# Kernel optimization log

Hardware: AMD Instinct MI355X
Metric: run time of the kernel (lower is better)

## Reference

```python
import jax, jax.numpy as jnp
import numpy as np

N, E, D, H = 50000, 640000, 128, 8
d = D // H  # per-head dim


def layernorm(x, g, b, eps=1e-5):
    mu = jnp.mean(x, axis=-1, keepdims=True)
    var = jnp.var(x, axis=-1, keepdims=True)
    return (x - mu) * jax.lax.rsqrt(var + eps) * g + b


def setup_inputs() -> dict:
    key = jax.random.key(0)
    ks = jax.random.split(key, 14)
    s = 0.05
    return {
        "node_emb": jax.random.normal(ks[0], (N, D), jnp.float32),
        "bond_emb": jax.random.normal(ks[1], (E, D), jnp.float32),
        "basic_attn": jax.random.uniform(ks[2], (E,), jnp.float32),
        "src": jax.random.randint(ks[3], (E,), 0, N),
        "dst": jax.random.randint(ks[4], (E,), 0, N),
        "Wk": jax.random.normal(ks[5], (D, D), jnp.float32) * s,
        "Wq": jax.random.normal(ks[6], (D, D), jnp.float32) * s,
        "Wv": jax.random.normal(ks[7], (D, D), jnp.float32) * s,
        "W_dis": jax.random.normal(ks[8], (1, H), jnp.float32) * s,
        "W_beta": jax.random.normal(ks[9], (3 * D, 1), jnp.float32) * s,
        "ln1_g": jnp.ones((D,), jnp.float32),
        "ln1_b": jnp.zeros((D,), jnp.float32),
        "W_ff1": jax.random.normal(ks[10], (D, 2 * D), jnp.float32) * s,
        "W_ff2": jax.random.normal(ks[11], (2 * D, D), jnp.float32) * s,
    }


def reference(node_emb, bond_emb, basic_attn, src, dst, Wk, Wq, Wv, W_dis,
              W_beta, ln1_g, ln1_b, W_ff1, W_ff2):
    n = node_emb.shape[0]
    # Q/K/V projections (eval mode: dropouts are identity)
    k = (node_emb @ Wk).reshape(n, H, d)
    q = (node_emb @ Wq).reshape(n, H, d)
    v = (bond_emb @ Wv).reshape(-1, H, d)          # per-edge values [E,H,d]
    # per-edge dot-product score (fn.u_dot_v) scaled by sqrt(out_feat)
    scores = jnp.einsum('ehd,ehd->eh', k[src], q[dst])
    scores = scores / jnp.sqrt(jnp.asarray(d, scores.dtype))
    # learned distance decay: Linear(1,H) on basic_attn
    dist = basic_attn[:, None] @ W_dis             # [E,H]
    logits = scores + dist
    # edge_softmax over in-edges of each destination node, per head
    mx = jax.ops.segment_max(logits, dst, num_segments=n)
    mx = jnp.where(jnp.isfinite(mx), mx, 0.0)
    e = jnp.exp(logits - mx[dst])
    den = jax.ops.segment_sum(e, dst, num_segments=n)
    att = e / (den[dst] + 1e-16)                   # [E,H]
    # message = v * att, scatter-sum to destination nodes
    ft = jax.ops.segment_sum(v * att[:, :, None], dst, num_segments=n)
    he = ft.reshape(n, D)
    # beta gating
    beta = jax.nn.sigmoid(
        jnp.concatenate([he, node_emb, he - node_emb], axis=-1) @ W_beta)
    he = beta * node_emb + (1.0 - beta) * he
    # FFN with pre-LN and identity-initialized post-LN
    h = layernorm(he, ln1_g, ln1_b)
    out = jax.nn.relu(h @ W_ff1) @ W_ff2
    ones = jnp.ones((D,), he.dtype)
    zeros = jnp.zeros((D,), he.dtype)
    return layernorm(out + he, ones, zeros)
```

## Files before the change

kernel.cpp:

```cpp
#include <hip/hip_runtime.h>
#include <math.h>

#define NN 50000
#define NE 640000
#define DIM 128
#define NH 8

typedef unsigned short u16;
typedef __attribute__((ext_vector_type(8))) short short8;
typedef __attribute__((ext_vector_type(4))) float f32x4;

__device__ __forceinline__ float wave_sum64(float v) {
  #pragma unroll
  for (int m = 32; m >= 1; m >>= 1) v += __shfl_xor(v, m, 64);
  return v;
}
__device__ __forceinline__ unsigned bf16pk(float a, float b) {
  unsigned ua = __float_as_uint(a); ua = (ua + 0x7fffu + ((ua >> 16) & 1u)) >> 16;
  unsigned ub = __float_as_uint(b); ub = (ub + 0x7fffu + ((ub >> 16) & 1u)) & 0xffff0000u;
  return ua | ub;
}
__device__ __forceinline__ u16 bf16c(float x) {
  unsigned u = __float_as_uint(x);
  return (u16)((u + 0x7fffu + ((u >> 16) & 1u)) >> 16);
}
__device__ __forceinline__ float bf_lo(unsigned v) { return __uint_as_float(v << 16); }
__device__ __forceinline__ float bf_hi(unsigned v) { return __uint_as_float(v & 0xffff0000u); }

#define AS1(p) ((const __attribute__((address_space(1))) unsigned*)(p))
#define AS3(p) ((__attribute__((address_space(3))) unsigned*)(p))

__global__ __launch_bounds__(256) void csr_count_k(const int* __restrict__ dst,
                                                   int* __restrict__ deg) {
  int e = blockIdx.x * 256 + threadIdx.x;
  if (e < NE) atomicAdd(&deg[dst[e]], 1);
}

#define SCAN_T 1024
#define SCHUNK 49
__global__ __launch_bounds__(1024) void scan_k(const int* __restrict__ deg,
                                               int* __restrict__ off,
                                               int* __restrict__ cursor) {
  __shared__ int part[SCAN_T];
  int t = threadIdx.x;
  int lo = t * SCHUNK, hi = lo + SCHUNK; if (hi > NN) hi = NN;
  int s = 0;
  for (int i = lo; i < hi; ++i) s += deg[i];
  part[t] = s;
  __syncthreads();
  for (int o = 1; o < SCAN_T; o <<= 1) {
    int v = (t >= o) ? part[t - o] : 0;
    __syncthreads();
    part[t] += v;
    __syncthreads();
  }
  int base = (t == 0) ? 0 : part[t - 1];
  for (int i = lo; i < hi; ++i) {
    off[i] = base; cursor[i] = base; base += deg[i];
  }
  if (t == SCAN_T - 1) off[NN] = part[SCAN_T - 1];
}

__global__ __launch_bounds__(256) void csr_fill_k(const int* __restrict__ dst,
                                                  int* __restrict__ cursor,
                                                  int* __restrict__ eids,
                                                  int* __restrict__ perm) {
  int e = blockIdx.x * 256 + threadIdx.x;
  if (e < NE) {
    int p = atomicAdd(&cursor[dst[e]], 1);
    eids[p] = e;
    perm[e] = p;
  }
}

__global__ __launch_bounds__(256) void cvt_node_k(const float* __restrict__ x,
                                                  unsigned* __restrict__ o) {
  int t = blockIdx.x * 256 + threadIdx.x;
  if (t < NN * 64) {
    float2 v = *(const float2*)(x + (size_t)2 * t);
    o[t] = bf16pk(v.x, v.y);
  }
}

__global__ __launch_bounds__(256) void wprep_k(const float* __restrict__ W,
                                               u16* __restrict__ Wt,
                                               int K, int N) {
  int t = blockIdx.x * 256 + threadIdx.x;
  if (t < K * N) {
    int n = t / K, k = t - n * K;
    Wt[t] = bf16c(W[(size_t)k * N + n]);
  }
}

__global__ __launch_bounds__(256) void qk_mfma_k(
    const u16* __restrict__ A, const u16* __restrict__ Wtq,
    const u16* __restrict__ Wtk, u16* __restrict__ qo,
    u16* __restrict__ ko) {
  __shared__ u16 At[64 * 128];
  const int wid = threadIdx.x >> 6, l = threadIdx.x & 63;
  const int quad = l >> 4, l16 = l & 15;
  const int c0 = (wid & 1) * 64;
  const u16* wt = (wid < 2) ? Wtq : Wtk;
  u16* ob = (wid < 2) ? qo : ko;
  short8 bfr[4][4];
  #pragma unroll
  for (int ct = 0; ct < 4; ++ct)
    #pragma unroll
    for (int ks = 0; ks < 4; ++ks)
      bfr[ct][ks] = *(const short8*)(wt + (c0 + ct * 16 + l16) * 128 + ks * 32 + quad * 8);
  const int ntiles = (NN + 63) / 64;
  for (int t = blockIdx.x; t < ntiles; t += gridDim.x) {
    const char* gsrc = (const char*)A + (size_t)t * 64 * 128 * 2;
    #pragma unroll
    for (int i = 0; i < 4; ++i) {
      int off = wid * 4096 + i * 1024;
      __builtin_amdgcn_global_load_lds(AS1(gsrc + off + l * 16),
                                       AS3((char*)At + off), 16, 0, 0);
    }
    __syncthreads();
    f32x4 acc[4][4];
    #pragma unroll
    for (int rt = 0; rt < 4; ++rt)
      #pragma unroll
      for (int ct = 0; ct < 4; ++ct)
        acc[rt][ct] = (f32x4){0.f, 0.f, 0.f, 0.f};
    #pragma unroll
    for (int ks = 0; ks < 4; ++ks) {
      short8 af[4];
      #pragma unroll
      for (int rt = 0; rt < 4; ++rt)
        af[rt] = *(const short8*)(At + (rt * 16 + l16) * 128 + ks * 32 + quad * 8);
      #pragma unroll
      for (int rt = 0; rt < 4; ++rt)
        #pragma unroll
        for (int ct = 0; ct < 4; ++ct)
          acc[rt][ct] = __builtin_amdgcn_mfma_f32_16x16x32_bf16(
              af[rt], bfr[ct][ks], acc[rt][ct], 0, 0, 0);
    }
    __syncthreads();
    #pragma unroll
    for (int rt = 0; rt < 4; ++rt)
      #pragma unroll
      for (int r = 0; r < 4; ++r) {
        int row = t * 64 + rt * 16 + quad * 4 + r;
        if (row < NN) {
          u16* op = ob + (size_t)row * 128 + c0 + l16;
          #pragma unroll
          for (int ct = 0; ct < 4; ++ct) op[ct * 16] = bf16c(acc[rt][ct][r]);
        }
      }
  }
}

__global__ __launch_bounds__(256) void ff1_mfma_k(
    const u16* __restrict__ A, const u16* __restrict__ Wt,
    u16* __restrict__ O) {
  __shared__ u16 At[64 * 128];
  const int wid = threadIdx.x >> 6, l = threadIdx.x & 63;
  const int quad = l >> 4, l16 = l & 15;
  const int c0 = wid * 64;
  short8 bfr[4][4];
  #pragma unroll
  for (int ct = 0; ct < 4; ++ct)
    #pragma unroll
    for (int ks = 0; ks < 4; ++ks)
      bfr[ct][ks] = *(const short8*)(Wt + (c0 + ct * 16 + l16) * 128 + ks * 32 + quad * 8);
  const int ntiles = (NN + 63) / 64;
  for (int t = blockIdx.x; t < ntiles; t += gridDim.x) {
    const char* gsrc = (const char*)A + (size_t)t * 64 * 128 * 2;
    #pragma unroll
    for (int i = 0; i < 4; ++i) {
      int off = wid * 4096 + i * 1024;
      __builtin_amdgcn_global_load_lds(AS1(gsrc + off + l * 16),
                                       AS3((char*)At + off), 16, 0, 0);
    }
    __syncthreads();
    f32x4 acc[4][4];
    #pragma unroll
    for (int rt = 0; rt < 4; ++rt)
      #pragma unroll
      for (int ct = 0; ct < 4; ++ct)
        acc[rt][ct] = (f32x4){0.f, 0.f, 0.f, 0.f};
    #pragma unroll
    for (int ks = 0; ks < 4; ++ks) {
      short8 af[4];
      #pragma unroll
      for (int rt = 0; rt < 4; ++rt)
        af[rt] = *(const short8*)(At + (rt * 16 + l16) * 128 + ks * 32 + quad * 8);
      #pragma unroll
      for (int rt = 0; rt < 4; ++rt)
        #pragma unroll
        for (int ct = 0; ct < 4; ++ct)
          acc[rt][ct] = __builtin_amdgcn_mfma_f32_16x16x32_bf16(
              af[rt], bfr[ct][ks], acc[rt][ct], 0, 0, 0);
    }
    __syncthreads();
    #pragma unroll
    for (int rt = 0; rt < 4; ++rt)
      #pragma unroll
      for (int r = 0; r < 4; ++r) {
        int row = t * 64 + rt * 16 + quad * 4 + r;
        if (row < NN) {
          u16* op = O + (size_t)row * 256 + c0 + l16;
          #pragma unroll
          for (int ct = 0; ct < 4; ++ct)
            op[ct * 16] = bf16c(fmaxf(acc[rt][ct][r], 0.f));
        }
      }
  }
}

__global__ __launch_bounds__(256) void ff2_mfma_k(
    const u16* __restrict__ A, const u16* __restrict__ Wt,
    const float* __restrict__ he, float* __restrict__ Z) {
  __shared__ u16 At[64 * 256];
  const int wid = threadIdx.x >> 6, l = threadIdx.x & 63;
  const int quad = l >> 4, l16 = l & 15;
  const int c0 = wid * 32;
  short8 bfr[2][8];
  #pragma unroll
  for (int ct = 0; ct < 2; ++ct)
    #pragma unroll
    for (int ks = 0; ks < 8; ++ks)
      bfr[ct][ks] = *(const short8*)(Wt + (c0 + ct * 16 + l16) * 256 + ks * 32 + quad * 8);
  const int ntiles = (NN + 63) / 64;
  for (int t = blockIdx.x; t < ntiles; t += gridDim.x) {
    const char* gsrc = (const char*)A + (size_t)t * 64 * 256 * 2;
    #pragma unroll
    for (int i = 0; i < 8; ++i) {
      int off = wid * 8192 + i * 1024;
      __builtin_amdgcn_global_load_lds(AS1(gsrc + off + l * 16),
                                       AS3((char*)At + off), 16, 0, 0);
    }
    __syncthreads();
    f32x4 acc[4][2];
    #pragma unroll
    for (int rt = 0; rt < 4; ++rt)
      #pragma unroll
      for (int ct = 0; ct < 2; ++ct)
        acc[rt][ct] = (f32x4){0.f, 0.f, 0.f, 0.f};
    #pragma unroll
    for (int ks = 0; ks < 8; ++ks) {
      short8 af[4];
      #pragma unroll
      for (int rt = 0; rt < 4; ++rt)
        af[rt] = *(const short8*)(At + (rt * 16 + l16) * 256 + ks * 32 + quad * 8);
      #pragma unroll
      for (int rt = 0; rt < 4; ++rt)
        #pragma unroll
        for (int ct = 0; ct < 2; ++ct)
          acc[rt][ct] = __builtin_amdgcn_mfma_f32_16x16x32_bf16(
              af[rt], bfr[ct][ks], acc[rt][ct], 0, 0, 0);
    }
    __syncthreads();
    #pragma unroll
    for (int rt = 0; rt < 4; ++rt)
      #pragma unroll
      for (int r = 0; r < 4; ++r) {
        int row = t * 64 + rt * 16 + quad * 4 + r;
        if (row < NN) {
          #pragma unroll
          for (int ct = 0; ct < 2; ++ct) {
            size_t idx = (size_t)row * 128 + c0 + ct * 16 + l16;
            Z[idx] = acc[rt][ct][r] + he[idx];
          }
        }
      }
  }
}

__global__ __launch_bounds__(256) void edge_logits_k(
    const unsigned* __restrict__ kb16, const unsigned* __restrict__ qb16,
    const float* __restrict__ ba, const int* __restrict__ src,
    const int* __restrict__ dst, const float* __restrict__ Wdis,
    const int* __restrict__ perm, float* __restrict__ exs) {
  int idx = blockIdx.x * 256 + threadIdx.x;
  if (idx >= NE * NH) return;
  int e = idx >> 3, h = idx & 7;
  int s = src[e], t = dst[e];
  const uint4* kp = (const uint4*)(kb16 + (size_t)s * 64 + h * 8);
  const uint4* qp = (const uint4*)(qb16 + (size_t)t * 64 + h * 8);
  uint4 A0 = kp[0], A1 = kp[1];
  uint4 B0 = qp[0], B1 = qp[1];
  float sc = 0.f;
  sc = fmaf(bf_lo(A0.x), bf_lo(B0.x), sc); sc = fmaf(bf_hi(A0.x), bf_hi(B0.x), sc);
  sc = fmaf(bf_lo(A0.y), bf_lo(B0.y), sc); sc = fmaf(bf_hi(A0.y), bf_hi(B0.y), sc);
  sc = fmaf(bf_lo(A0.z), bf_lo(B0.z), sc); sc = fmaf(bf_hi(A0.z), bf_hi(B0.z), sc);
  sc = fmaf(bf_lo(A0.w), bf_lo(B0.w), sc); sc = fmaf(bf_hi(A0.w), bf_hi(B0.w), sc);
  sc = fmaf(bf_lo(A1.x), bf_lo(B1.x), sc); sc = fmaf(bf_hi(A1.x), bf_hi(B1.x), sc);
  sc = fmaf(bf_lo(A1.y), bf_lo(B1.y), sc); sc = fmaf(bf_hi(A1.y), bf_hi(B1.y), sc);
  sc = fmaf(bf_lo(A1.z), bf_lo(B1.z), sc); sc = fmaf(bf_hi(A1.z), bf_hi(B1.z), sc);
  sc = fmaf(bf_lo(A1.w), bf_lo(B1.w), sc); sc = fmaf(bf_hi(A1.w), bf_hi(B1.w), sc);
  exs[(size_t)perm[e] * 8 + h] = __expf(sc * 0.25f + ba[e] * Wdis[h]);
}

__global__ __launch_bounds__(512, 6) void node_attn_k(
    const float* __restrict__ bond, const float* __restrict__ WvG,
    const float* __restrict__ exs, const int* __restrict__ off,
    const int* __restrict__ eids, const float* __restrict__ x,
    const float* __restrict__ Wb, const float* __restrict__ g1,
    const float* __restrict__ b1, float* __restrict__ he,
    unsigned* __restrict__ hbuf16) {
  __shared__ unsigned Wvpk[DIM * 64];
  __shared__ unsigned gbuf[8][NH][67];
  for (int t = threadIdx.x; t < DIM * 64; t += 512) {
    int i = t >> 6, c = t & 63;
    Wvpk[t] = bf16pk(WvG[i * DIM + c], WvG[i * DIM + c + 64]);
  }
  __syncthreads();
  const int wid = threadIdx.x >> 6, l = threadIdx.x & 63;
  const int hh = l & 7;
  const float wb0 = Wb[l],         wb1 = Wb[l + 64];
  const float wb2 = Wb[DIM + l],   wb3 = Wb[DIM + l + 64];
  const float wb4 = Wb[2*DIM + l], wb5 = Wb[2*DIM + l + 64];
  const float gl0 = g1[l], gl1 = g1[l + 64];
  const float bl0 = b1[l], bl1 = b1[l + 64];

  for (int n = blockIdx.x * 8 + wid; n < NN; n += gridDim.x * 8) {
    int o0 = __builtin_amdgcn_readfirstlane(off[n]);
    int o1 = __builtin_amdgcn_readfirstlane(off[n + 1]);
    int deg = o1 - o0;
    float acc[16];
    #pragma unroll
    for (int i = 0; i < 16; ++i) acc[i] = 0.f;

    float dsum = 0.f;
    for (int p = o0 * 8 + l; p < o1 * 8; p += 64) dsum += exs[p];
    dsum += __shfl_xor(dsum, 8, 64);
    dsum += __shfl_xor(dsum, 16, 64);
    dsum += __shfl_xor(dsum, 32, 64);
    float rden = 1.f / (dsum + 1e-16f);

    for (int g = 0; g < deg; g += 8) {
      float2 bc[8];
      #pragma unroll
      for (int s = 0; s < 8; ++s) {
        if (g + s < deg) {
          int e = eids[o0 + g + s];
          bc[s] = *(const float2*)(bond + (size_t)e * DIM + 2 * l);
        }
      }
      #pragma unroll
      for (int s = 0; s < 8; ++s) {
        if (g + s < deg) {
          const float4* ep = (const float4*)(exs) + (size_t)(o0 + g + s) * 2;
          float4 ea = ep[0], eb = ep[1];
          float2 bv = bc[s];
          acc[0]  = fmaf(ea.x, bv.x, acc[0]);  acc[1]  = fmaf(ea.x, bv.y, acc[1]);
          acc[2]  = fmaf(ea.y, bv.x, acc[2]);  acc[3]  = fmaf(ea.y, bv.y, acc[3]);
          acc[4]  = fmaf(ea.z, bv.x, acc[4]);  acc[5]  = fmaf(ea.z, bv.y, acc[5]);
          acc[6]  = fmaf(ea.w, bv.x, acc[6]);  acc[7]  = fmaf(ea.w, bv.y, acc[7]);
          acc[8]  = fmaf(eb.x, bv.x, acc[8]);  acc[9]  = fmaf(eb.x, bv.y, acc[9]);
          acc[10] = fmaf(eb.y, bv.x, acc[10]); acc[11] = fmaf(eb.y, bv.y, acc[11]);
          acc[12] = fmaf(eb.z, bv.x, acc[12]); acc[13] = fmaf(eb.z, bv.y, acc[13]);
          acc[14] = fmaf(eb.w, bv.x, acc[14]); acc[15] = fmaf(eb.w, bv.y, acc[15]);
        }
      }
    }
    #pragma unroll
    for (int h = 0; h < 8; ++h) {
      float rh = __shfl(rden, h, 64);
      acc[2 * h] *= rh; acc[2 * h + 1] *= rh;
    }
    #pragma unroll
    for (int h = 0; h < 8; ++h)
      gbuf[wid][h][l] = bf16pk(acc[2 * h], acc[2 * h + 1]);
    int h0 = l >> 4, h1 = 4 + (l >> 4);
    float f0 = 0.f, f1 = 0.f;
    #pragma unroll 8
    for (int ii = 0; ii < 64; ++ii) {
      unsigned u = gbuf[wid][h0][ii];
      unsigned v = gbuf[wid][h1][ii];
      unsigned w0 = Wvpk[(2 * ii) * 64 + l];
      unsigned w1 = Wvpk[(2 * ii + 1) * 64 + l];
      f0 = fmaf(bf_lo(u), bf_lo(w0), f0); f0 = fmaf(bf_hi(u), bf_lo(w1), f0);
      f1 = fmaf(bf_lo(v), bf_hi(w0), f1); f1 = fmaf(bf_hi(v), bf_hi(w1), f1);
    }
    float x0 = x[(size_t)n * DIM + l], x1 = x[(size_t)n * DIM + l + 64];
    float s = f0 * wb0 + x0 * wb2 + (f0 - x0) * wb4
            + f1 * wb1 + x1 * wb3 + (f1 - x1) * wb5;
    s = wave_sum64(s);
    float beta = 1.f / (1.f + __expf(-s));
    float he0 = beta * x0 + (1.f - beta) * f0;
    float he1 = beta * x1 + (1.f - beta) * f1;
    he[(size_t)n * DIM + l] = he0;
    he[(size_t)n * DIM + l + 64] = he1;
    float mu = wave_sum64(he0 + he1) * (1.f / DIM);
    float vr = wave_sum64(he0 * he0 + he1 * he1) * (1.f / DIM) - mu * mu;
    float rs = rsqrtf(vr + 1e-5f);
    float v0 = (he0 - mu) * rs * gl0 + bl0;
    float v1 = (he1 - mu) * rs * gl1 + bl1;
    int i0 = (2 * l) & 63, i1 = (2 * l + 1) & 63;
    float a0 = __shfl(v0, i0, 64), b0 = __shfl(v1, i0, 64);
    float a1 = __shfl(v0, i1, 64), b1v = __shfl(v1, i1, 64);
    float c0 = (l < 32) ? a0 : b0;
    float c1 = (l < 32) ? a1 : b1v;
    hbuf16[(size_t)n * 64 + l] = bf16pk(c0, c1);
  }
}

__global__ __launch_bounds__(256) void ln_out_k(const float* __restrict__ z,
                                                float* __restrict__ outp) {
  const int wid = threadIdx.x >> 6, l = threadIdx.x & 63;
  int n = blockIdx.x * 4 + wid;
  if (n >= NN) return;
  float z0 = z[(size_t)n * DIM + l];
  float z1 = z[(size_t)n * DIM + l + 64];
  float mu = wave_sum64(z0 + z1) * (1.f / DIM);
  float vr = wave_sum64(z0 * z0 + z1 * z1) * (1.f / DIM) - mu * mu;
  float rs = rsqrtf(vr + 1e-5f);
  outp[(size_t)n * DIM + l]      = (z0 - mu) * rs;
  outp[(size_t)n * DIM + l + 64] = (z1 - mu) * rs;
}

extern "C" void kernel_launch(void* const* d_in, const int* in_sizes, int n_in,
                              void* d_out, int out_size, void* d_ws, size_t ws_size,
                              hipStream_t stream) {
  const float* node = (const float*)d_in[0];
  const float* bond = (const float*)d_in[1];
  const float* ba   = (const float*)d_in[2];
  const int*   src  = (const int*)  d_in[3];
  const int*   dst  = (const int*)  d_in[4];
  const float* Wk   = (const float*)d_in[5];
  const float* Wq   = (const float*)d_in[6];
  const float* Wv   = (const float*)d_in[7];
  const float* Wdis = (const float*)d_in[8];
  const float* Wb   = (const float*)d_in[9];
  const float* g1   = (const float*)d_in[10];
  const float* b1   = (const float*)d_in[11];
  const float* W1   = (const float*)d_in[12];
  const float* W2   = (const float*)d_in[13];
  float* out = (float*)d_out;

  char* W = (char*)d_ws;
  u16* node16 = (u16*)(W);
  u16* qb16   = (u16*)(W + 13000000);
  u16* hid16  = (u16*)(W);
  u16* kb16   = (u16*)(W + 26000000);
  u16* hbuf16 = (u16*)(W + 26000000);
  float* exs  = (float*)(W + 39000000);
  int* perm   = (int*)(W + 59500000);
  float* z    = (float*)(W + 39000000);
  float* he   = (float*)(W + 64600000);
  u16* Wtq    = (u16*)(W + 90200000);
  u16* Wtk    = Wtq + 128 * 128;
  u16* Wt1    = Wtk + 128 * 128;
  u16* Wt2    = Wt1 + 256 * 128;
  int* deg    = (int*)(W + 90400000);
  int* off    = deg + (NN + 1);
  int* cursor = off + (NN + 1);
  int* eids   = cursor + (NN + 1);

  hipMemsetAsync(deg, 0, (size_t)(NN + 1) * 4, stream);

  csr_count_k<<<(NE + 255) / 256, 256, 0, stream>>>(dst, deg);
  scan_k<<<1, 1024, 0, stream>>>(deg, off, cursor);
  csr_fill_k<<<(NE + 255) / 256, 256, 0, stream>>>(dst, cursor, eids, perm);

  cvt_node_k<<<(NN * 64 + 255) / 256, 256, 0, stream>>>(node, (unsigned*)node16);
  wprep_k<<<(128 * 128 + 255) / 256, 256, 0, stream>>>(Wq, Wtq, 128, 128);
  wprep_k<<<(128 * 128 + 255) / 256, 256, 0, stream>>>(Wk, Wtk, 128, 128);
  wprep_k<<<(256 * 128 + 255) / 256, 256, 0, stream>>>(W1, Wt1, 128, 256);
  wprep_k<<<(256 * 128 + 255) / 256, 256, 0, stream>>>(W2, Wt2, 256, 128);

  const int ntiles = (NN + 63) / 64;

  qk_mfma_k<<<ntiles, 256, 0, stream>>>(node16, Wtq, Wtk, qb16, kb16);

  edge_logits_k<<<(NE * NH + 255) / 256, 256, 0, stream>>>(
      (const unsigned*)kb16, (const unsigned*)qb16, ba, src, dst, Wdis, perm, exs);

  node_attn_k<<<3125, 512, 0, stream>>>(bond, Wv, exs, off, eids, node,
                                        Wb, g1, b1, he, (unsigned*)hbuf16);

  ff1_mfma_k<<<ntiles, 256, 0, stream>>>(hbuf16, Wt1, hid16);
  ff2_mfma_k<<<ntiles, 256, 0, stream>>>(hid16, Wt2, he, z);
  ln_out_k<<<(NN + 3) / 4, 256, 0, stream>>>(z, out);
}
```

Baseline: 851.9 us.

## Fuse prep kernels, FFN+LN, swizzle LDS, and drop perm scatter in edge pass

Merges node conversion, weight transposes and degree counting into one prep kernel. Fuses FF1, FF2, the residual and the final layernorm into a single kernel that keeps the hidden tile in LDS, and XOR-swizzles LDS tiles to reduce bank conflicts. The edge pass now iterates in CSR order via eids, so the perm array goes away. The softmax denominator is accumulated inside the main aggregation loop instead of in a separate pass. The cost is more LDS per block and gathered reads of src/dst/ba through eids.

```diff
diff --git a/kernel.cpp b/kernel.cpp
--- a/kernel.cpp
+++ b/kernel.cpp
@@ -30,10 +30,38 @@
 #define AS1(p) ((const __attribute__((address_space(1))) unsigned*)(p))
 #define AS3(p) ((__attribute__((address_space(3))) unsigned*)(p))
 
-__global__ __launch_bounds__(256) void csr_count_k(const int* __restrict__ dst,
-                                                   int* __restrict__ deg) {
-  int e = blockIdx.x * 256 + threadIdx.x;
-  if (e < NE) atomicAdd(&deg[dst[e]], 1);
+__global__ __launch_bounds__(256) void prep_k(
+    const float* __restrict__ node, unsigned* __restrict__ node16,
+    const float* __restrict__ Wq, const float* __restrict__ Wk,
+    const float* __restrict__ W1, const float* __restrict__ W2,
+    u16* __restrict__ Wtq, u16* __restrict__ Wtk,
+    u16* __restrict__ Wt1, u16* __restrict__ Wt2,
+    const int* __restrict__ dst, int* __restrict__ deg) {
+  int b = blockIdx.x, tid = threadIdx.x;
+  if (b < 12500) {
+    int t = b * 256 + tid;
+    float2 v = *(const float2*)(node + (size_t)2 * t);
+    node16[t] = bf16pk(v.x, v.y);
+  } else if (b < 12564) {
+    int t = (b - 12500) * 256 + tid;
+    int n = t >> 7, k = t & 127;
+    Wtq[t] = bf16c(Wq[(size_t)k * 128 + n]);
+  } else if (b < 12628) {
+    int t = (b - 12564) * 256 + tid;
+    int n = t >> 7, k = t & 127;
+    Wtk[t] = bf16c(Wk[(size_t)k * 128 + n]);
+  } else if (b < 12756) {
+    int t = (b - 12628) * 256 + tid;
+    int n = t >> 7, k = t & 127;
+    Wt1[t] = bf16c(W1[(size_t)k * 256 + n]);
+  } else if (b < 12884) {
+    int t = (b - 12756) * 256 + tid;
+    int n = t >> 8, k = t & 255;
+    Wt2[t] = bf16c(W2[(size_t)k * 128 + n]);
+  } else {
+    int e = (b - 12884) * 256 + tid;
+    atomicAdd(&deg[dst[e]], 1);
+  }
 }
 
 #define SCAN_T 1024
@@ -63,32 +91,11 @@
 
 __global__ __launch_bounds__(256) void csr_fill_k(const int* __restrict__ dst,
                                                   int* __restrict__ cursor,
-                                                  int* __restrict__ eids,
-                                                  int* __restrict__ perm) {
+                                                  int* __restrict__ eids) {
   int e = blockIdx.x * 256 + threadIdx.x;
   if (e < NE) {
     int p = atomicAdd(&cursor[dst[e]], 1);
     eids[p] = e;
-    perm[e] = p;
-  }
-}
-
-__global__ __launch_bounds__(256) void cvt_node_k(const float* __restrict__ x,
-                                                  unsigned* __restrict__ o) {
-  int t = blockIdx.x * 256 + threadIdx.x;
-  if (t < NN * 64) {
-    float2 v = *(const float2*)(x + (size_t)2 * t);
-    o[t] = bf16pk(v.x, v.y);
-  }
-}
-
-__global__ __launch_bounds__(256) void wprep_k(const float* __restrict__ W,
-                                               u16* __restrict__ Wt,
-                                               int K, int N) {
-  int t = blockIdx.x * 256 + threadIdx.x;
-  if (t < K * N) {
-    int n = t / K, k = t - n * K;
-    Wt[t] = bf16c(W[(size_t)k * N + n]);
   }
 }
 
@@ -113,9 +120,10 @@
     const char* gsrc = (const char*)A + (size_t)t * 64 * 128 * 2;
     #pragma unroll
     for (int i = 0; i < 4; ++i) {
-      int off = wid * 4096 + i * 1024;
-      __builtin_amdgcn_global_load_lds(AS1(gsrc + off + l * 16),
-                                       AS3((char*)At + off), 16, 0, 0);
+      int dbase = wid * 4096 + i * 1024;
+      int soff = (dbase + l * 16) ^ ((((i * 4) + (l >> 4)) & 7) << 4);
+      __builtin_amdgcn_global_load_lds(AS1(gsrc + soff),
+                                       AS3((char*)At + dbase), 16, 0, 0);
     }
     __syncthreads();
     f32x4 acc[4][4];
@@ -128,8 +136,10 @@
     for (int ks = 0; ks < 4; ++ks) {
       short8 af[4];
       #pragma unroll
-      for (int rt = 0; rt < 4; ++rt)
-        af[rt] = *(const short8*)(At + (rt * 16 + l16) * 128 + ks * 32 + quad * 8);
+      for (int rt = 0; rt < 4; ++rt) {
+        int bo = (((rt * 16 + l16) * 128 + ks * 32 + quad * 8) * 2) ^ ((l16 & 7) << 4);
+        af[rt] = *(const short8*)((const char*)At + bo);
+      }
       #pragma unroll
       for (int rt = 0; rt < 4; ++rt)
         #pragma unroll
@@ -152,131 +162,146 @@
   }
 }
 
-__global__ __launch_bounds__(256) void ff1_mfma_k(
-    const u16* __restrict__ A, const u16* __restrict__ Wt,
-    u16* __restrict__ O) {
-  __shared__ u16 At[64 * 128];
+__global__ __launch_bounds__(256) void ffn_mfma_k(
+    const u16* __restrict__ A, const u16* __restrict__ Wt1,
+    const u16* __restrict__ Wt2, const float* __restrict__ he,
+    float* __restrict__ outp) {
+  __shared__ __align__(16) u16 At[64 * 128];
+  __shared__ __align__(16) u16 Ht[64 * 256];
+  __shared__ float redS[4][64], redQ[4][64];
   const int wid = threadIdx.x >> 6, l = threadIdx.x & 63;
   const int quad = l >> 4, l16 = l & 15;
-  const int c0 = wid * 64;
-  short8 bfr[4][4];
-  #pragma unroll
-  for (int ct = 0; ct < 4; ++ct)
-    #pragma unroll
-    for (int ks = 0; ks < 4; ++ks)
-      bfr[ct][ks] = *(const short8*)(Wt + (c0 + ct * 16 + l16) * 128 + ks * 32 + quad * 8);
+  const int c1 = wid * 64;
+  const int c2 = wid * 32;
   const int ntiles = (NN + 63) / 64;
   for (int t = blockIdx.x; t < ntiles; t += gridDim.x) {
+    short8 b1f[4][4];
+    #pragma unroll
+    for (int ct = 0; ct < 4; ++ct)
+      #pragma unroll
+      for (int ks = 0; ks < 4; ++ks)
+        b1f[ct][ks] = *(const short8*)(Wt1 + (c1 + ct * 16 + l16) * 128 + ks * 32 + quad * 8);
     const char* gsrc = (const char*)A + (size_t)t * 64 * 128 * 2;
     #pragma unroll
     for (int i = 0; i < 4; ++i) {
-      int off = wid * 4096 + i * 1024;
-      __builtin_amdgcn_global_load_lds(AS1(gsrc + off + l * 16),
-                                       AS3((char*)At + off), 16, 0, 0);
-    }
-    __syncthreads();
-    f32x4 acc[4][4];
+      int dbase = wid * 4096 + i * 1024;
+      int soff = (dbase + l * 16) ^ ((((i * 4) + (l >> 4)) & 7) << 4);
+      __builtin_amdgcn_global_load_lds(AS1(gsrc + soff),
+                                       AS3((char*)At + dbase), 16, 0, 0);
+    }
+    __syncthreads();
+    f32x4 acc1[4][4];
     #pragma unroll
     for (int rt = 0; rt < 4; ++rt)
       #pragma unroll
       for (int ct = 0; ct < 4; ++ct)
-        acc[rt][ct] = (f32x4){0.f, 0.f, 0.f, 0.f};
+        acc1[rt][ct] = (f32x4){0.f, 0.f, 0.f, 0.f};
     #pragma unroll
     for (int ks = 0; ks < 4; ++ks) {
       short8 af[4];
       #pragma unroll
-      for (int rt = 0; rt < 4; ++rt)
-        af[rt] = *(const short8*)(At + (rt * 16 + l16) * 128 + ks * 32 + quad * 8);
+      for (int rt = 0; rt < 4; ++rt) {
+        int bo = (((rt * 16 + l16) * 128 + ks * 32 + quad * 8) * 2) ^ ((l16 & 7) << 4);
+        af[rt] = *(const short8*)((const char*)At + bo);
+      }
       #pragma unroll
       for (int rt = 0; rt < 4; ++rt)
         #pragma unroll
         for (int ct = 0; ct < 4; ++ct)
-          acc[rt][ct] = __builtin_amdgcn_mfma_f32_16x16x32_bf16(
-              af[rt], bfr[ct][ks], acc[rt][ct], 0, 0, 0);
-    }
-    __syncthreads();
+          acc1[rt][ct] = __builtin_amdgcn_mfma_f32_16x16x32_bf16(
+              af[rt], b1f[ct][ks], acc1[rt][ct], 0, 0, 0);
+    }
     #pragma unroll
     for (int rt = 0; rt < 4; ++rt)
       #pragma unroll
       for (int r = 0; r < 4; ++r) {
-        int row = t * 64 + rt * 16 + quad * 4 + r;
-        if (row < NN) {
-          u16* op = O + (size_t)row * 256 + c0 + l16;
-          #pragma unroll
-          for (int ct = 0; ct < 4; ++ct)
-            op[ct * 16] = bf16c(fmaxf(acc[rt][ct][r], 0.f));
-        }
-      }
-  }
-}
-
-__global__ __launch_bounds__(256) void ff2_mfma_k(
-    const u16* __restrict__ A, const u16* __restrict__ Wt,
-    const float* __restrict__ he, float* __restrict__ Z) {
-  __shared__ u16 At[64 * 256];
-  const int wid = threadIdx.x >> 6, l = threadIdx.x & 63;
-  const int quad = l >> 4, l16 = l & 15;
-  const int c0 = wid * 32;
-  short8 bfr[2][8];
-  #pragma unroll
-  for (int ct = 0; ct < 2; ++ct)
-    #pragma unroll
-    for (int ks = 0; ks < 8; ++ks)
-      bfr[ct][ks] = *(const short8*)(Wt + (c0 + ct * 16 + l16) * 256 + ks * 32 + quad * 8);
-  const int ntiles = (NN + 63) / 64;
-  for (int t = blockIdx.x; t < ntiles; t += gridDim.x) {
-    const char* gsrc = (const char*)A + (size_t)t * 64 * 256 * 2;
-    #pragma unroll
-    for (int i = 0; i < 8; ++i) {
-      int off = wid * 8192 + i * 1024;
-      __builtin_amdgcn_global_load_lds(AS1(gsrc + off + l * 16),
-                                       AS3((char*)At + off), 16, 0, 0);
-    }
-    __syncthreads();
-    f32x4 acc[4][2];
+        int row = rt * 16 + quad * 4 + r;
+        #pragma unroll
+        for (int ct = 0; ct < 4; ++ct) {
+          int col = c1 + ct * 16 + l16;
+          int bo = (row * 512 + col * 2) ^ ((row & 7) << 4);
+          *(u16*)((char*)Ht + bo) = bf16c(fmaxf(acc1[rt][ct][r], 0.f));
+        }
+      }
+    __syncthreads();
+    short8 b2f[2][8];
+    #pragma unroll
+    for (int ct = 0; ct < 2; ++ct)
+      #pragma unroll
+      for (int ks = 0; ks < 8; ++ks)
+        b2f[ct][ks] = *(const short8*)(Wt2 + (c2 + ct * 16 + l16) * 256 + ks * 32 + quad * 8);
+    f32x4 acc2[4][2];
     #pragma unroll
     for (int rt = 0; rt < 4; ++rt)
       #pragma unroll
       for (int ct = 0; ct < 2; ++ct)
-        acc[rt][ct] = (f32x4){0.f, 0.f, 0.f, 0.f};
+        acc2[rt][ct] = (f32x4){0.f, 0.f, 0.f, 0.f};
     #pragma unroll
     for (int ks = 0; ks < 8; ++ks) {
       short8 af[4];
       #pragma unroll
-      for (int rt = 0; rt < 4; ++rt)
-        af[rt] = *(const short8*)(At + (rt * 16 + l16) * 256 + ks * 32 + quad * 8);
+      for (int rt = 0; rt < 4; ++rt) {
+        int bo = ((rt * 16 + l16) * 512 + ks * 64 + quad * 16) ^ ((l16 & 7) << 4);
+        af[rt] = *(const short8*)((const char*)Ht + bo);
+      }
       #pragma unroll
       for (int rt = 0; rt < 4; ++rt)
         #pragma unroll
         for (int ct = 0; ct < 2; ++ct)
-          acc[rt][ct] = __builtin_amdgcn_mfma_f32_16x16x32_bf16(
-              af[rt], bfr[ct][ks], acc[rt][ct], 0, 0, 0);
-    }
-    __syncthreads();
+          acc2[rt][ct] = __builtin_amdgcn_mfma_f32_16x16x32_bf16(
+              af[rt], b2f[ct][ks], acc2[rt][ct], 0, 0, 0);
+    }
     #pragma unroll
     for (int rt = 0; rt < 4; ++rt)
       #pragma unroll
       for (int r = 0; r < 4; ++r) {
-        int row = t * 64 + rt * 16 + quad * 4 + r;
-        if (row < NN) {
-          #pragma unroll
-          for (int ct = 0; ct < 2; ++ct) {
-            size_t idx = (size_t)row * 128 + c0 + ct * 16 + l16;
-            Z[idx] = acc[rt][ct][r] + he[idx];
-          }
-        }
-      }
-  }
-}
-
-__global__ __launch_bounds__(256) void edge_logits_k(
+        int row = rt * 16 + quad * 4 + r;
+        int grow = t * 64 + row;
+        float h0 = 0.f, h1 = 0.f;
+        if (grow < NN) {
+          h0 = he[(size_t)grow * 128 + c2 + l16];
+          h1 = he[(size_t)grow * 128 + c2 + 16 + l16];
+        }
+        float z0 = acc2[rt][0][r] + h0;
+        float z1 = acc2[rt][1][r] + h1;
+        acc2[rt][0][r] = z0; acc2[rt][1][r] = z1;
+        float ps = z0 + z1;
+        float pq = fmaf(z0, z0, z1 * z1);
+        ps += __shfl_xor(ps, 1, 64);  pq += __shfl_xor(pq, 1, 64);
+        ps += __shfl_xor(ps, 2, 64);  pq += __shfl_xor(pq, 2, 64);
+        ps += __shfl_xor(ps, 4, 64);  pq += __shfl_xor(pq, 4, 64);
+        ps += __shfl_xor(ps, 8, 64);  pq += __shfl_xor(pq, 8, 64);
+        if (l16 == 0) { redS[wid][row] = ps; redQ[wid][row] = pq; }
+      }
+    __syncthreads();
+    #pragma unroll
+    for (int rt = 0; rt < 4; ++rt)
+      #pragma unroll
+      for (int r = 0; r < 4; ++r) {
+        int row = rt * 16 + quad * 4 + r;
+        int grow = t * 64 + row;
+        float s4 = redS[0][row] + redS[1][row] + redS[2][row] + redS[3][row];
+        float q4 = redQ[0][row] + redQ[1][row] + redQ[2][row] + redQ[3][row];
+        float mu = s4 * (1.f / 128.f);
+        float vr = q4 * (1.f / 128.f) - mu * mu;
+        float rs = rsqrtf(vr + 1e-5f);
+        if (grow < NN) {
+          outp[(size_t)grow * 128 + c2 + l16]      = (acc2[rt][0][r] - mu) * rs;
+          outp[(size_t)grow * 128 + c2 + 16 + l16] = (acc2[rt][1][r] - mu) * rs;
+        }
+      }
+  }
+}
+
+__global__ __launch_bounds__(256) void edge_exp_k(
     const unsigned* __restrict__ kb16, const unsigned* __restrict__ qb16,
     const float* __restrict__ ba, const int* __restrict__ src,
     const int* __restrict__ dst, const float* __restrict__ Wdis,
-    const int* __restrict__ perm, float* __restrict__ exs) {
+    const int* __restrict__ eids, float* __restrict__ exs) {
   int idx = blockIdx.x * 256 + threadIdx.x;
   if (idx >= NE * NH) return;
-  int e = idx >> 3, h = idx & 7;
+  int p = idx >> 3, h = idx & 7;
+  int e = eids[p];
   int s = src[e], t = dst[e];
   const uint4* kp = (const uint4*)(kb16 + (size_t)s * 64 + h * 8);
   const uint4* qp = (const uint4*)(qb16 + (size_t)t * 64 + h * 8);
@@ -291,7 +316,7 @@
   sc = fmaf(bf_lo(A1.y), bf_lo(B1.y), sc); sc = fmaf(bf_hi(A1.y), bf_hi(B1.y), sc);
   sc = fmaf(bf_lo(A1.z), bf_lo(B1.z), sc); sc = fmaf(bf_hi(A1.z), bf_hi(B1.z), sc);
   sc = fmaf(bf_lo(A1.w), bf_lo(B1.w), sc); sc = fmaf(bf_hi(A1.w), bf_hi(B1.w), sc);
-  exs[(size_t)perm[e] * 8 + h] = __expf(sc * 0.25f + ba[e] * Wdis[h]);
+  exs[idx] = __expf(sc * 0.25f + ba[e] * Wdis[h]);
 }
 
 __global__ __launch_bounds__(512, 6) void node_attn_k(
@@ -323,13 +348,8 @@
     float acc[16];
     #pragma unroll
     for (int i = 0; i < 16; ++i) acc[i] = 0.f;
-
-    float dsum = 0.f;
-    for (int p = o0 * 8 + l; p < o1 * 8; p += 64) dsum += exs[p];
-    dsum += __shfl_xor(dsum, 8, 64);
-    dsum += __shfl_xor(dsum, 16, 64);
-    dsum += __shfl_xor(dsum, 32, 64);
-    float rden = 1.f / (dsum + 1e-16f);
+    float d0 = 0.f, d1 = 0.f, d2 = 0.f, d3 = 0.f;
+    float d4 = 0.f, d5 = 0.f, d6 = 0.f, d7 = 0.f;
 
     for (int g = 0; g < deg; g += 8) {
       float2 bc[8];
@@ -345,6 +365,8 @@
         if (g + s < deg) {
           const float4* ep = (const float4*)(exs) + (size_t)(o0 + g + s) * 2;
           float4 ea = ep[0], eb = ep[1];
+          d0 += ea.x; d1 += ea.y; d2 += ea.z; d3 += ea.w;
+          d4 += eb.x; d5 += eb.y; d6 += eb.z; d7 += eb.w;
           float2 bv = bc[s];
           acc[0]  = fmaf(ea.x, bv.x, acc[0]);  acc[1]  = fmaf(ea.x, bv.y, acc[1]);
           acc[2]  = fmaf(ea.y, bv.x, acc[2]);  acc[3]  = fmaf(ea.y, bv.y, acc[3]);
@@ -357,6 +379,11 @@
         }
       }
     }
+    float dsa = (hh & 1) ? d1 : d0, dsb = (hh & 1) ? d3 : d2;
+    float dsc = (hh & 1) ? d5 : d4, dsd = (hh & 1) ? d7 : d6;
+    float dse = (hh & 2) ? dsb : dsa, dsf = (hh & 2) ? dsd : dsc;
+    float dsel = (hh & 4) ? dsf : dse;
+    float rden = 1.f / (dsel + 1e-16f);
     #pragma unroll
     for (int h = 0; h < 8; ++h) {
       float rh = __shfl(rden, h, 64);
@@ -399,20 +426,6 @@
   }
 }
 
-__global__ __launch_bounds__(256) void ln_out_k(const float* __restrict__ z,
-                                                float* __restrict__ outp) {
-  const int wid = threadIdx.x >> 6, l = threadIdx.x & 63;
-  int n = blockIdx.x * 4 + wid;
-  if (n >= NN) return;
-  float z0 = z[(size_t)n * DIM + l];
-  float z1 = z[(size_t)n * DIM + l + 64];
-  float mu = wave_sum64(z0 + z1) * (1.f / DIM);
-  float vr = wave_sum64(z0 * z0 + z1 * z1) * (1.f / DIM) - mu * mu;
-  float rs = rsqrtf(vr + 1e-5f);
-  outp[(size_t)n * DIM + l]      = (z0 - mu) * rs;
-  outp[(size_t)n * DIM + l + 64] = (z1 - mu) * rs;
-}
-
 extern "C" void kernel_launch(void* const* d_in, const int* in_sizes, int n_in,
                               void* d_out, int out_size, void* d_ws, size_t ws_size,
                               hipStream_t stream) {
@@ -435,12 +448,9 @@
   char* W = (char*)d_ws;
   u16* node16 = (u16*)(W);
   u16* qb16   = (u16*)(W + 13000000);
-  u16* hid16  = (u16*)(W);
   u16* kb16   = (u16*)(W + 26000000);
   u16* hbuf16 = (u16*)(W + 26000000);
   float* exs  = (float*)(W + 39000000);
-  int* perm   = (int*)(W + 59500000);
-  float* z    = (float*)(W + 39000000);
   float* he   = (float*)(W + 64600000);
   u16* Wtq    = (u16*)(W + 90200000);
   u16* Wtk    = Wtq + 128 * 128;
@@ -453,27 +463,20 @@
 
   hipMemsetAsync(deg, 0, (size_t)(NN + 1) * 4, stream);
 
-  csr_count_k<<<(NE + 255) / 256, 256, 0, stream>>>(dst, deg);
+  prep_k<<<15384, 256, 0, stream>>>(node, (unsigned*)node16, Wq, Wk, W1, W2,
+                                    Wtq, Wtk, Wt1, Wt2, dst, deg);
   scan_k<<<1, 1024, 0, stream>>>(deg, off, cursor);
-  csr_fill_k<<<(NE + 255) / 256, 256, 0, stream>>>(dst, cursor, eids, perm);
-
-  cvt_node_k<<<(NN * 64 + 255) / 256, 256, 0, stream>>>(node, (unsigned*)node16);
-  wprep_k<<<(128 * 128 + 255) / 256, 256, 0, stream>>>(Wq, Wtq, 128, 128);
-  wprep_k<<<(128 * 128 + 255) / 256, 256, 0, stream>>>(Wk, Wtk, 128, 128);
-  wprep_k<<<(256 * 128 + 255) / 256, 256, 0, stream>>>(W1, Wt1, 128, 256);
-  wprep_k<<<(256 * 128 + 255) / 256, 256, 0, stream>>>(W2, Wt2, 256, 128);
+  csr_fill_k<<<(NE + 255) / 256, 256, 0, stream>>>(dst, cursor, eids);
 
   const int ntiles = (NN + 63) / 64;
 
   qk_mfma_k<<<ntiles, 256, 0, stream>>>(node16, Wtq, Wtk, qb16, kb16);
 
-  edge_logits_k<<<(NE * NH + 255) / 256, 256, 0, stream>>>(
-      (const unsigned*)kb16, (const unsigned*)qb16, ba, src, dst, Wdis, perm, exs);
+  edge_exp_k<<<(NE * NH + 255) / 256, 256, 0, stream>>>(
+      (const unsigned*)kb16, (const unsigned*)qb16, ba, src, dst, Wdis, eids, exs);
 
   node_attn_k<<<3125, 512, 0, stream>>>(bond, Wv, exs, off, eids, node,
                                         Wb, g1, b1, he, (unsigned*)hbuf16);
 
-  ff1_mfma_k<<<ntiles, 256, 0, stream>>>(hbuf16, Wt1, hid16);
-  ff2_mfma_k<<<ntiles, 256, 0, stream>>>(hid16, Wt2, he, z);
-  ln_out_k<<<(NN + 3) / 4, 256, 0, stream>>>(z, out);
-}
+  ffn_mfma_k<<<ntiles, 256, 0, stream>>>(hbuf16, Wt1, Wt2, he, out);
+}
```

Result: no change. 858.6 us (+0.8%).
